# Kernel optimization log

Measured on AMD Instinct MI355X. Metric: run time of the kernel, lower is better.

The kernel has to match this reference:

```python
import jax, jax.numpy as jnp
import numpy as np
from jax import lax

SL, BS, D, H, T = 256, 64, 1024, 512, 17
BN_EPS = 1e-5


def setup_inputs() -> dict:
    key = jax.random.key(0)
    ks = jax.random.split(key, 16)
    k = 1.0 / np.sqrt(H)
    u = lambda kk, shape: jax.random.uniform(kk, shape, jnp.float32, -k, k)
    word_input = jax.random.normal(ks[0], (SL, BS, D), jnp.float32)
    lengths = jax.random.randint(ks[1], (BS,), SL // 2, SL + 1)
    mask = jnp.arange(SL)[:, None] < lengths[None, :]  # (SL, BS), first step all valid
    labels = jax.random.randint(ks[2], (SL, BS), 0, T)
    return dict(
        word_input=word_input, mask=mask, labels=labels,
        w_ih_f=u(ks[3], (4 * H, D)), w_hh_f=u(ks[4], (4 * H, H)),
        b_ih_f=u(ks[5], (4 * H,)), b_hh_f=u(ks[6], (4 * H,)),
        w_ih_b=u(ks[7], (4 * H, D)), w_hh_b=u(ks[8], (4 * H, H)),
        b_ih_b=u(ks[9], (4 * H,)), b_hh_b=u(ks[10], (4 * H,)),
        bn_gamma=jnp.ones((2 * H,), jnp.float32), bn_beta=jnp.zeros((2 * H,), jnp.float32),
        lin_w=u(ks[11], (T, 2 * H)), lin_b=u(ks[12], (T,)),
        crf_start=0.1 * jax.random.normal(ks[13], (T,), jnp.float32),
        crf_end=0.1 * jax.random.normal(ks[14], (T,), jnp.float32),
        crf_trans=0.1 * jax.random.normal(ks[15], (T, T), jnp.float32),
    )


def _lstm_dir(x, w_ih, w_hh, b_ih, b_hh, reverse):
    # x: (SL, BS, D); PyTorch gate order i, f, g, o
    B = x.shape[1]
    h0 = jnp.zeros((B, H), x.dtype)
    xg = jnp.einsum('sbd,gd->sbg', x, w_ih) + b_ih + b_hh  # precompute input projections

    def step(carry, xt):
        h, c = carry
        g = xt + h @ w_hh.T
        i, f, gg, o = jnp.split(g, 4, axis=-1)
        c = jax.nn.sigmoid(f) * c + jax.nn.sigmoid(i) * jnp.tanh(gg)
        h = jax.nn.sigmoid(o) * jnp.tanh(c)
        return (h, c), h

    _, hs = lax.scan(step, (h0, h0), xg, reverse=reverse)
    return hs  # (SL, BS, H)


def _crf_llh(E, y, m, start, end, trans):
    # E: (B, L, T) batch-first emissions; y: (B, L) int; m: (B, L) bool
    B = E.shape[0]
    mf = m.astype(E.dtype)
    b = jnp.arange(B)
    # numerator (gold path score)
    emit = jnp.take_along_axis(E, y[:, :, None], axis=2)[:, :, 0]  # (B, L)
    num = start[y[:, 0]] + emit[:, 0]
    tr = trans[y[:, :-1], y[:, 1:]]  # (B, L-1)
    num = num + jnp.sum(mf[:, 1:] * (tr + emit[:, 1:]), axis=1)
    last = jnp.sum(m.astype(jnp.int32), axis=1) - 1
    num = num + end[y[b, last]]
    # partition function via forward algorithm
    alpha0 = start + E[:, 0]  # (B, T)

    def step(alpha, inp):
        e_t, m_t = inp
        nxt = jax.nn.logsumexp(alpha[:, :, None] + trans[None], axis=1) + e_t
        return jnp.where(m_t[:, None], nxt, alpha), None

    alpha, _ = lax.scan(step, alpha0, (E[:, 1:].transpose(1, 0, 2), m[:, 1:].T))
    Z = jax.nn.logsumexp(alpha + end, axis=1)
    return jnp.sum(num - Z)


def _viterbi(E, m, start, end, trans):
    # E: (B, L, T); m: (B, L) bool -> padded tags (B, L)
    B = E.shape[0]
    b = jnp.arange(B)
    score0 = start + E[:, 0]  # (B, T)

    def fwd(score, inp):
        e_t, m_t = inp
        cand = score[:, :, None] + trans[None]  # (B, T, T)
        best_prev = jnp.argmax(cand, axis=1)  # (B, T)
        best = jnp.max(cand, axis=1) + e_t
        return jnp.where(m_t[:, None], best, score), best_prev

    final, history = lax.scan(fwd, score0, (E[:, 1:].transpose(1, 0, 2), m[:, 1:].T))
    last_tag = jnp.argmax(final + end, axis=1)  # (B,)

    def bwd(tag, inp):
        bp, m_t = inp
        prev = jnp.where(m_t, bp[b, tag], tag)
        return prev, tag

    tag0, tags_rest = lax.scan(bwd, last_tag, (history, m[:, 1:].T), reverse=True)
    tags = jnp.concatenate([tag0[None], tags_rest], axis=0).T  # (B, L)
    return jnp.where(m, tags, 0)


def _forward(word_input, mask, labels, w_ih_f, w_hh_f, b_ih_f, b_hh_f,
             w_ih_b, w_hh_b, b_ih_b, b_hh_b, bn_gamma, bn_beta, lin_w, lin_b,
             crf_start, crf_end, crf_trans):
    hf = _lstm_dir(word_input, w_ih_f, w_hh_f, b_ih_f, b_hh_f, reverse=False)
    hb = _lstm_dir(word_input, w_ih_b, w_hh_b, b_ih_b, b_hh_b, reverse=True)
    lstm_out = jnp.concatenate([hf, hb], axis=-1)  # (SL, BS, 2H)
    x = lstm_out.reshape(-1, 2 * H)
    mean = x.mean(0)
    var = x.var(0)  # biased, as in torch BN training normalization
    xn = (x - mean) / jnp.sqrt(var + BN_EPS) * bn_gamma + bn_beta
    logits = xn @ lin_w.T + lin_b  # (SL*BS, T)
    E = logits.reshape(SL, BS, T).transpose(1, 0, 2)  # batch-first (B, L, T)
    m = mask.T  # (B, L)
    loss = -_crf_llh(E, labels.T, m, crf_start, crf_end, crf_trans)
    preds = _viterbi(E, m, crf_start, crf_end, crf_trans)
    return loss, preds


def reference(word_input, mask, labels, w_ih_f, w_hh_f, b_ih_f, b_hh_f,
              w_ih_b, w_hh_b, b_ih_b, b_hh_b, bn_gamma, bn_beta, lin_w, lin_b,
              crf_start, crf_end, crf_trans):
    return _forward(word_input, mask, labels, w_ih_f, w_hh_f, b_ih_f, b_hh_f,
                    w_ih_b, w_hh_b, b_ih_b, b_hh_b, bn_gamma, bn_beta, lin_w, lin_b,
                    crf_start, crf_end, crf_trans)
```

## Files before the change

### kernel.cpp

```cpp
#include <hip/hip_runtime.h>
#include <hip/hip_bf16.h>
#include <math.h>

#define SL 256
#define BS 64
#define DI 1024
#define HH 512
#define TT 17
#define NR (SL*BS)
#define G4 (4*HH)
#define C2 (2*HH)
#define NBLK 128

__device__ __forceinline__ float sigm(float x) { return 1.f / (1.f + expf(-x)); }

typedef float vfloat4 __attribute__((ext_vector_type(4)));
typedef __attribute__((ext_vector_type(8))) short short8v;
typedef __attribute__((ext_vector_type(4))) float f32x4;

__device__ __forceinline__ void coh_load4(float4& d, const float* p) {
    asm volatile("global_load_dwordx4 %0, %1, off sc0 sc1" : "=v"(d) : "v"(p) : "memory");
}
__device__ __forceinline__ void coh_load4i(int4& d, const int* p) {
    asm volatile("global_load_dwordx4 %0, %1, off sc0 sc1" : "=v"(d) : "v"(p) : "memory");
}
__device__ __forceinline__ void coh_store4(const float4& d, float* p) {
    vfloat4 t; t.x = d.x; t.y = d.y; t.z = d.z; t.w = d.w;
    asm volatile("global_store_dwordx4 %0, %1, off sc0 sc1" :: "v"(p), "v"(t) : "memory");
}
__device__ __forceinline__ void wait_vm0() { asm volatile("s_waitcnt vmcnt(0)" ::: "memory"); }

__device__ __forceinline__ void split8(const float4& x0, const float4& x1,
                                       short8v& h, short8v& l)
{
    const float xs[8] = {x0.x, x0.y, x0.z, x0.w, x1.x, x1.y, x1.z, x1.w};
    #pragma unroll
    for (int j = 0; j < 8; ++j) {
        const uint u   = __float_as_uint(xs[j]);
        const float hf = __uint_as_float(u & 0xFFFF0000u);
        h[j] = (short)(u >> 16);
        const float lo = xs[j] - hf;
        const uint v   = __float_as_uint(lo);
        l[j] = (short)((v + 0x7FFFu + ((v >> 16) & 1u)) >> 16);
    }
}

__global__ __launch_bounds__(256) void gemm_xg_mfma(
    const float* __restrict__ A,
    const float* __restrict__ W,
    const float* __restrict__ b1,
    const float* __restrict__ b2,
    float* __restrict__ C)
{
    const int tid  = threadIdx.x;
    const int lane = tid & 63;
    const int w    = tid >> 6;
    const int wm   = w >> 1, wn = w & 1;
    const int m0   = blockIdx.y * 128 + wm * 64;
    const int n0   = blockIdx.x * 128 + wn * 64;
    const int lr   = lane & 15;
    const int lk   = (lane >> 4) * 8;

    const float* pA = A + (size_t)(m0 + lr) * DI + lk;
    const float* pB = W + (size_t)(n0 + lr) * DI + lk;

    f32x4 acc[4][4];
    #pragma unroll
    for (int i = 0; i < 4; i++)
        #pragma unroll
        for (int j = 0; j < 4; j++) {
            acc[i][j][0] = 0.f; acc[i][j][1] = 0.f;
            acc[i][j][2] = 0.f; acc[i][j][3] = 0.f;
        }

    for (int k0 = 0; k0 < DI; k0 += 32) {
        short8v ah[4], al[4], bh[4], bl[4];
        #pragma unroll
        for (int i = 0; i < 4; i++) {
            const float4 a0 = *(const float4*)(pA + (size_t)i * 16 * DI + k0);
            const float4 a1 = *(const float4*)(pA + (size_t)i * 16 * DI + k0 + 4);
            split8(a0, a1, ah[i], al[i]);
            const float4 b0 = *(const float4*)(pB + (size_t)i * 16 * DI + k0);
            const float4 b1v = *(const float4*)(pB + (size_t)i * 16 * DI + k0 + 4);
            split8(b0, b1v, bh[i], bl[i]);
        }
        #pragma unroll
        for (int i = 0; i < 4; i++)
            #pragma unroll
            for (int j = 0; j < 4; j++)
                acc[i][j] = __builtin_amdgcn_mfma_f32_16x16x32_bf16(ah[i], bh[j], acc[i][j], 0, 0, 0);
        #pragma unroll
        for (int i = 0; i < 4; i++)
            #pragma unroll
            for (int j = 0; j < 4; j++)
                acc[i][j] = __builtin_amdgcn_mfma_f32_16x16x32_bf16(ah[i], bl[j], acc[i][j], 0, 0, 0);
        #pragma unroll
        for (int i = 0; i < 4; i++)
            #pragma unroll
            for (int j = 0; j < 4; j++)
                acc[i][j] = __builtin_amdgcn_mfma_f32_16x16x32_bf16(al[i], bh[j], acc[i][j], 0, 0, 0);
    }

    #pragma unroll
    for (int j = 0; j < 4; j++) {
        const int n  = n0 + j * 16 + lr;
        const float bs = b1[n] + b2[n];
        const int u  = n & 511, g = n >> 9;
        const int s0 = u >> 2,  c = g * 4 + (u & 3);
        #pragma unroll
        for (int i = 0; i < 4; i++) {
            #pragma unroll
            for (int r = 0; r < 4; r++) {
                const int m  = m0 + i * 16 + (lane >> 4) * 4 + r;
                const int mt = m >> 6, mb = m & 63;
                C[((((size_t)s0 * SL + mt) * BS + mb) << 4) + c] = acc[i][j][r] + bs;
            }
        }
    }
}

__global__ __launch_bounds__(256) void pack_whh_v3(const float* __restrict__ whh,
                                                   float* __restrict__ wp)
{
    const int s = blockIdx.x;
    for (int idx = threadIdx.x; idx < 512 * 24; idx += 256) {
        const int k = idx / 24, c = idx % 24;
        float v = 0.f;
        if (c < 16) {
            const int g = c >> 2, uu = c & 3;
            v = whh[(size_t)(g * 512 + 4 * s + uu) * HH + k];
        }
        wp[(size_t)s * 12288 + idx] = v;
    }
}

__global__ __launch_bounds__(512) void init_flags(int* __restrict__ f)
{
    f[blockIdx.x * 512 + threadIdx.x] = 0;
}

__global__ __launch_bounds__(512, 2) void lstm_flag(
    const float* __restrict__ xg_f, const float* __restrict__ xg_b,
    const float* __restrict__ wp_f, const float* __restrict__ wp_b,
    float* __restrict__ Hf, float* __restrict__ Hb,
    int* __restrict__ flag_f, int* __restrict__ flag_b,
    float* __restrict__ out,
    int dir_base)
{
    __shared__ float w_s[512 * 24];
    __shared__ float hs[128 * 68];
    __shared__ float g_s[16 * 65];
    __shared__ float hpub[256];
    float* const part = hs;

    const int dir = dir_base + (blockIdx.x >> 7);
    const int s   = blockIdx.x & 127;
    const float* xg  = dir ? xg_b : xg_f;
    const float* wp  = dir ? wp_b : wp_f;
    float* Hbuf      = dir ? Hb : Hf;
    int*   flag      = dir ? flag_b : flag_f;
    const int reverse = dir;
    const int col_off = dir * HH;

    const int tid = threadIdx.x;
    const int ks  = tid >> 4;
    const int bt  = (tid >> 1) & 7;
    const int ct  = tid & 1;
    const int wv  = tid >> 6;

    {
        const float4* src = (const float4*)(wp + (size_t)s * 12288);
        float4* dst = (float4*)w_s;
        for (int i = tid; i < 3072; i += 512) dst[i] = src[i];
    }

    const float* xgs = xg + (size_t)s * (SL * 1024);
    float cst = 0.f;
    float4 r[4];
    float4 acc[8][2];

    for (int step = 0; step < SL; ++step) {
        const int t = reverse ? (SL - 1 - step) : step;
        const float myxg0 = xgs[t * 1024 + tid];
        const float myxg1 = xgs[t * 1024 + 512 + tid];

        if (step > 0) {
            if (tid < 32) {
                const int* fp = flag + (step - 1) * NBLK + tid * 4;
                int4 f;
                for (;;) {
                    coh_load4i(f, fp);
                    wait_vm0();
                    if (f.x & f.y & f.z & f.w) break;
                    __builtin_amdgcn_s_sleep(1);
                }
            }
            __syncthreads();

            const float* hsrc = Hbuf + ((step + 1) & 1) * (512 * 64);
            #pragma unroll
            for (int i = 0; i < 4; ++i)
                coh_load4(r[i], hsrc + (size_t)(i * 512 + tid) * 4);

            #pragma unroll
            for (int i = 0; i < 8; ++i) {
                acc[i][0] = make_float4(0.f, 0.f, 0.f, 0.f);
                acc[i][1] = make_float4(0.f, 0.f, 0.f, 0.f);
            }

            for (int kc = 0; kc < 4; ++kc) {
                if (kc) __syncthreads();
                wait_vm0();
                #pragma unroll
                for (int i = 0; i < 4; ++i) {
                    const int idx = i * 512 + tid;
                    const int k = idx >> 4, b4 = (idx & 15) * 4;
                    *(float4*)&hs[k * 68 + b4] = r[i];
                }
                __syncthreads();
                if (kc < 3) {
                    const float* base = hsrc + (size_t)(kc + 1) * 8192;
                    #pragma unroll
                    for (int i = 0; i < 4; ++i)
                        coh_load4(r[i], base + (size_t)(i * 512 + tid) * 4);
                }
                #pragma unroll
                for (int j = 0; j < 4; ++j) {
                    const int kk = ks + 32 * j;
                    const int kg = kc * 128 + kk;
                    const float4 w0 = *(const float4*)&w_s[kg * 24 + ct * 8];
                    const float4 w1 = *(const float4*)&w_s[kg * 24 + ct * 8 + 4];
                    const float* hp = &hs[kk * 68 + 8 * bt];
                    const float2 h01 = *(const float2*)(hp + 0);
                    const float2 h23 = *(const float2*)(hp + 2);
                    const float2 h45 = *(const float2*)(hp + 4);
                    const float2 h67 = *(const float2*)(hp + 6);
                    const float hv[8] = {h01.x, h01.y, h23.x, h23.y, h45.x, h45.y, h67.x, h67.y};
                    #pragma unroll
                    for (int i = 0; i < 8; ++i) {
                        acc[i][0].x = fmaf(hv[i], w0.x, acc[i][0].x);
                        acc[i][0].y = fmaf(hv[i], w0.y, acc[i][0].y);
                        acc[i][0].z = fmaf(hv[i], w0.z, acc[i][0].z);
                        acc[i][0].w = fmaf(hv[i], w0.w, acc[i][0].w);
                        acc[i][1].x = fmaf(hv[i], w1.x, acc[i][1].x);
                        acc[i][1].y = fmaf(hv[i], w1.y, acc[i][1].y);
                        acc[i][1].z = fmaf(hv[i], w1.z, acc[i][1].z);
                        acc[i][1].w = fmaf(hv[i], w1.w, acc[i][1].w);
                    }
                }
            }
            #pragma unroll
            for (int i = 0; i < 8; ++i)
                #pragma unroll
                for (int p = 0; p < 2; ++p) {
                    acc[i][p].x += __shfl_xor(acc[i][p].x, 16);
                    acc[i][p].y += __shfl_xor(acc[i][p].y, 16);
                    acc[i][p].z += __shfl_xor(acc[i][p].z, 16);
                    acc[i][p].w += __shfl_xor(acc[i][p].w, 16);
                    acc[i][p].x += __shfl_xor(acc[i][p].x, 32);
                    acc[i][p].y += __shfl_xor(acc[i][p].y, 32);
                    acc[i][p].z += __shfl_xor(acc[i][p].z, 32);
                    acc[i][p].w += __shfl_xor(acc[i][p].w, 32);
                }
            __syncthreads();
            if ((tid & 63) < 16) {
                #pragma unroll
                for (int i = 0; i < 8; ++i) {
                    const int base = wv * 1088 + (8 * bt + i) * 16 + ct * 8 + bt * 8;
                    *(float4*)&part[base + 0] = acc[i][0];
                    *(float4*)&part[base + 4] = acc[i][1];
                }
            }
            __syncthreads();
        }

        {
            float v0 = myxg0, v1 = myxg1;
            if (step > 0) {
                const int gA = tid, gB = tid + 512;
                const int iA = gA + 8 * (gA >> 7);
                const int iB = gB + 8 * (gB >> 7);
                #pragma unroll
                for (int w = 0; w < 8; ++w) {
                    v0 += part[w * 1088 + iA];
                    v1 += part[w * 1088 + iB];
                }
            }
            g_s[(tid & 15) * 65 + (tid >> 4)] = v0;
            {
                const int gB = tid + 512;
                g_s[(gB & 15) * 65 + (gB >> 4)] = v1;
            }
        }
        __syncthreads();

        if (tid < 256) {
            const int b = tid & 63, uu = tid >> 6;
            const float ig = sigm(g_s[(0  + uu) * 65 + b]);
            const float fg = sigm(g_s[(4  + uu) * 65 + b]);
            const float gg = tanhf(g_s[(8  + uu) * 65 + b]);
            const float og = sigm(g_s[(12 + uu) * 65 + b]);
            cst = fg * cst + ig * gg;
            hpub[tid] = og * tanhf(cst);
        }
        __syncthreads();
        if (tid < 16) {
            const float4 v = *(const float4*)&hpub[tid * 16];
            coh_store4(v, Hbuf + (step & 1) * (512 * 64) + s * 256 + tid * 16);
            *(float4*)(out + (size_t)(col_off + 4 * s + (tid >> 2)) * NR
                           + (size_t)t * 64 + (tid & 3) * 16) = v;
        }
        if (wv == 0) wait_vm0();
        __syncthreads();
        if (tid == 0)
            __hip_atomic_store(flag + step * NBLK + s, 1,
                               __ATOMIC_RELEASE, __HIP_MEMORY_SCOPE_AGENT);
    }
}

__global__ __launch_bounds__(256) void bn_stats(
    const float* __restrict__ X2, float* __restrict__ mean, float* __restrict__ istd)
{
    const int ch = blockIdx.x, tid = threadIdx.x;
    const float* base = X2 + (size_t)ch * NR;
    __shared__ float red[256];
    float s = 0.f;
    for (int i = tid * 4; i < NR; i += 1024) {
        const float4 v = *(const float4*)(base + i);
        s += v.x + v.y + v.z + v.w;
    }
    red[tid] = s; __syncthreads();
    for (int o = 128; o; o >>= 1) { if (tid < o) red[tid] += red[tid + o]; __syncthreads(); }
    const float mu = red[0] * (1.f / NR);
    __syncthreads();
    float vv = 0.f;
    for (int i = tid * 4; i < NR; i += 1024) {
        const float4 v = *(const float4*)(base + i);
        const float d0 = v.x - mu, d1 = v.y - mu, d2 = v.z - mu, d3 = v.w - mu;
        vv += d0 * d0 + d1 * d1 + d2 * d2 + d3 * d3;
    }
    red[tid] = vv; __syncthreads();
    for (int o = 128; o; o >>= 1) { if (tid < o) red[tid] += red[tid + o]; __syncthreads(); }
    if (tid == 0) { mean[ch] = mu; istd[ch] = rsqrtf(red[0] * (1.f / NR) + 1e-5f); }
}

__global__ void fold_lin(const float* __restrict__ lin_w, const float* __restrict__ lin_b,
                         const float* __restrict__ gamma, const float* __restrict__ beta,
                         const float* __restrict__ mean, const float* __restrict__ istd,
                         float* __restrict__ Wf, float* __restrict__ ct)
{
    const int t = blockIdx.x, tid = threadIdx.x;
    __shared__ float red[256];
    float acc = 0.f;
    for (int cc = tid; cc < C2; cc += 256) {
        const float w = lin_w[t * C2 + cc];
        const float g = gamma[cc] * istd[cc];
        Wf[t * C2 + cc] = w * g;
        acc = fmaf(beta[cc] - mean[cc] * g, w, acc);
    }
    red[tid] = acc; __syncthreads();
    for (int o = 128; o; o >>= 1) { if (tid < o) red[tid] += red[tid + o]; __syncthreads(); }
    if (tid == 0) ct[t] = red[0] + lin_b[t];
}

__global__ __launch_bounds__(256) void emit_logits(
    const float* __restrict__ X2, const float* __restrict__ Wf,
    const float* __restrict__ ct, float* __restrict__ E)
{
    __shared__ float ps[256 * TT];
    const int t = blockIdx.x;
    const int tid = threadIdx.x;
    const int b = tid & 63, p = tid >> 6;
    const float* xb = X2 + (size_t)t * 64 + b;

    float acc[TT];
    #pragma unroll
    for (int k = 0; k < TT; k++) acc[k] = 0.f;

    for (int c0 = p * 256; c0 < p * 256 + 256; c0 += 4) {
        const float x0 = xb[(size_t)(c0 + 0) * NR];
        const float x1 = xb[(size_t)(c0 + 1) * NR];
        const float x2 = xb[(size_t)(c0 + 2) * NR];
        const float x3 = xb[(size_t)(c0 + 3) * NR];
        #pragma unroll
        for (int k = 0; k < TT; k++) {
            const float4 w = *(const float4*)&Wf[k * C2 + c0];
            acc[k] = fmaf(x0, w.x, fmaf(x1, w.y, fmaf(x2, w.z, fmaf(x3, w.w, acc[k]))));
        }
    }
    #pragma unroll
    for (int k = 0; k < TT; k++) ps[tid * TT + k] = acc[k];
    __syncthreads();
    if (tid < 64) {
        float* Er = E + ((size_t)tid * SL + t) * TT;
        #pragma unroll
        for (int k = 0; k < TT; k++) {
            float v = ct[k];
            #pragma unroll
            for (int q = 0; q < 4; q++) v += ps[(q * 64 + tid) * TT + k];
            Er[k] = v;
        }
    }
}

__global__ __launch_bounds__(64) void crf_llh(
    const float* __restrict__ E, const int* __restrict__ mask,
    const int* __restrict__ labels, const float* __restrict__ startv,
    const float* __restrict__ endv, const float* __restrict__ trans,
    float* __restrict__ res)
{
    const int b = blockIdx.x, lane = threadIdx.x;
    __shared__ float tr[TT][TT];
    for (int i = lane; i < TT * TT; i += 64) tr[i / TT][i % TT] = trans[i];
    __syncthreads();
    const float* Eb = E + (size_t)b * SL * TT;
    const int j = (lane < TT) ? lane : 0;

    float alpha = -1e30f;
    if (lane < TT) alpha = startv[lane] + Eb[lane];

    float numacc = 0.f; int len = 0;
    for (int t = lane; t < SL; t += 64) {
        const int mt = mask[t * BS + b];
        len += (mt != 0);
        if (t >= 1 && mt) {
            const int yp = labels[(t - 1) * BS + b];
            const int yt = labels[t * BS + b];
            numacc += tr[yp][yt] + Eb[t * TT + yt];
        }
    }
    for (int off = 32; off; off >>= 1) {
        numacc += __shfl_xor(numacc, off);
        len += __shfl_xor(len, off);
    }

    for (int t = 1; t < SL; ++t) {
        const int mt = mask[t * BS + b];
        if (mt) {
            float av[TT];
            #pragma unroll
            for (int i = 0; i < TT; i++) av[i] = __shfl(alpha, i);
            const float e = (lane < TT) ? Eb[t * TT + lane] : 0.f;
            float mx = -1e30f;
            #pragma unroll
            for (int i = 0; i < TT; i++) mx = fmaxf(mx, av[i] + tr[i][j]);
            float ssum = 0.f;
            #pragma unroll
            for (int i = 0; i < TT; i++) ssum += expf(av[i] + tr[i][j] - mx);
            const float nxt = mx + logf(ssum) + e;
            if (lane < TT) alpha = nxt;
        }
    }
    float v = (lane < TT) ? alpha + endv[lane] : -1e30f;
    float mx = v;
    for (int off = 32; off; off >>= 1) mx = fmaxf(mx, __shfl_xor(mx, off));
    float se = (lane < TT) ? expf(v - mx) : 0.f;
    for (int off = 32; off; off >>= 1) se += __shfl_xor(se, off);
    const float Z = mx + logf(se);

    if (lane == 0) {
        const int y0 = labels[b];
        float num = startv[y0] + Eb[y0] + numacc;
        const int last = len - 1;
        const int yl = labels[last * BS + b];
        num += endv[yl];
        res[b] = num - Z;
    }
}

__global__ __launch_bounds__(64) void loss_reduce(const float* __restrict__ res, float* __restrict__ out)
{
    const int lane = threadIdx.x;
    float v = res[lane];
    for (int off = 32; off; off >>= 1) v += __shfl_xor(v, off);
    if (lane == 0) out[0] = -v;
}

__global__ __launch_bounds__(64) void viterbi(
    const float* __restrict__ E, const int* __restrict__ mask,
    const float* __restrict__ startv, const float* __restrict__ endv,
    const float* __restrict__ trans, float* __restrict__ preds)
{
    const int b = blockIdx.x, lane = threadIdx.x;
    __shared__ float tr[TT][TT];
    __shared__ unsigned char bp[SL][TT];
    for (int i = lane; i < TT * TT; i += 64) tr[i / TT][i % TT] = trans[i];
    __syncthreads();
    const float* Eb = E + (size_t)b * SL * TT;
    const int j = (lane < TT) ? lane : 0;

    float score = (lane < TT) ? startv[lane] + Eb[lane] : -1e30f;
    for (int t = 1; t < SL; ++t) {
        float av[TT];
        #pragma unroll
        for (int i = 0; i < TT; i++) av[i] = __shfl(score, i);
        float best = -1e30f; int bi = 0;
        #pragma unroll
        for (int i = 0; i < TT; i++) {
            const float cand = av[i] + tr[i][j];
            if (cand > best) { best = cand; bi = i; }
        }
        const int mt = mask[t * BS + b];
        if (lane < TT) {
            bp[t][lane] = (unsigned char)bi;
            if (mt) score = best + Eb[t * TT + lane];
        }
    }
    float v = (lane < TT) ? score + endv[lane] : -1e30f;
    float mx = v;
    for (int off = 32; off; off >>= 1) mx = fmaxf(mx, __shfl_xor(mx, off));
    unsigned long long ball = __ballot(v == mx);
    const int last_tag = __ffsll(ball) - 1;
    __syncthreads();

    if (lane == 0) {
        int tag = last_tag;
        float* pb = preds + (size_t)b * SL;
        for (int t = SL - 1; t >= 1; --t) {
            const int mt = mask[t * BS + b];
            pb[t] = mt ? (float)tag : 0.f;
            if (mt) tag = bp[t][tag];
        }
        pb[0] = mask[b] ? (float)tag : 0.f;
    }
}

extern "C" void kernel_launch(void* const* d_in, const int* in_sizes, int n_in,
                              void* d_out, int out_size, void* d_ws, size_t ws_size,
                              hipStream_t stream)
{
    const float* word    = (const float*)d_in[0];
    const int*   mask    = (const int*)  d_in[1];
    const int*   labels  = (const int*)  d_in[2];
    const float* w_ih_f  = (const float*)d_in[3];
    const float* w_hh_f  = (const float*)d_in[4];
    const float* b_ih_f  = (const float*)d_in[5];
    const float* b_hh_f  = (const float*)d_in[6];
    const float* w_ih_b  = (const float*)d_in[7];
    const float* w_hh_b  = (const float*)d_in[8];
    const float* b_ih_b  = (const float*)d_in[9];
    const float* b_hh_b  = (const float*)d_in[10];
    const float* gamma   = (const float*)d_in[11];
    const float* beta    = (const float*)d_in[12];
    const float* lin_w   = (const float*)d_in[13];
    const float* lin_b   = (const float*)d_in[14];
    const float* c_start = (const float*)d_in[15];
    const float* c_end   = (const float*)d_in[16];
    const float* c_trans = (const float*)d_in[17];
    float* out = (float*)d_out;
    (void)in_sizes; (void)n_in; (void)out_size;

    char* ws = (char*)d_ws;
    size_t off = 0;
    auto alloc = [&](size_t bytes) {
        void* p = ws + off;
        off += (bytes + 255) & ~(size_t)255;
        return p;
    };
    float* XG_F  = (float*)alloc((size_t)NR * G4 * 4);
    float* WPK_F = (float*)alloc((size_t)128 * 12288 * 4);
    float* WPK_B = (float*)alloc((size_t)128 * 12288 * 4);
    float* LOUT  = (float*)alloc((size_t)NR * C2 * 4);
    float* HB_F  = (float*)alloc((size_t)2 * 512 * 64 * 4);
    float* HB_B  = (float*)alloc((size_t)2 * 512 * 64 * 4);
    int*   FLAGS = (int*)  alloc((size_t)2 * SL * NBLK * 4);
    float* MEAN  = (float*)alloc(C2 * 4);
    float* ISTD  = (float*)alloc(C2 * 4);
    float* WF    = (float*)alloc(TT * C2 * 4);
    float* CT    = (float*)alloc(TT * 4);
    float* Ebuf  = (float*)alloc((size_t)BS * SL * TT * 4);
    float* RES   = (float*)alloc(BS * 4);
    float* XG_B  = (float*)alloc((size_t)NR * G4 * 4);
    const bool merged = (ws_size >= off);
    if (!merged) XG_B = XG_F;

    init_flags<<<128, 512, 0, stream>>>(FLAGS);
    pack_whh_v3<<<128, 256, 0, stream>>>(w_hh_f, WPK_F);
    pack_whh_v3<<<128, 256, 0, stream>>>(w_hh_b, WPK_B);

    if (merged) {
        gemm_xg_mfma<<<dim3(G4 / 128, NR / 128), 256, 0, stream>>>(word, w_ih_f, b_ih_f, b_hh_f, XG_F);
        gemm_xg_mfma<<<dim3(G4 / 128, NR / 128), 256, 0, stream>>>(word, w_ih_b, b_ih_b, b_hh_b, XG_B);
        lstm_flag<<<2 * NBLK, 512, 0, stream>>>(XG_F, XG_B, WPK_F, WPK_B, HB_F, HB_B,
                                                FLAGS, FLAGS + SL * NBLK, LOUT, 0);
    } else {
        gemm_xg_mfma<<<dim3(G4 / 128, NR / 128), 256, 0, stream>>>(word, w_ih_f, b_ih_f, b_hh_f, XG_F);
        lstm_flag<<<NBLK, 512, 0, stream>>>(XG_F, XG_B, WPK_F, WPK_B, HB_F, HB_B,
                                            FLAGS, FLAGS + SL * NBLK, LOUT, 0);
        gemm_xg_mfma<<<dim3(G4 / 128, NR / 128), 256, 0, stream>>>(word, w_ih_b, b_ih_b, b_hh_b, XG_F);
        lstm_flag<<<NBLK, 512, 0, stream>>>(XG_F, XG_B, WPK_F, WPK_B, HB_F, HB_B,
                                            FLAGS, FLAGS + SL * NBLK, LOUT, 1);
    }

    bn_stats<<<C2, 256, 0, stream>>>(LOUT, MEAN, ISTD);
    fold_lin<<<TT, 256, 0, stream>>>(lin_w, lin_b, gamma, beta, MEAN, ISTD, WF, CT);
    emit_logits<<<SL, 256, 0, stream>>>(LOUT, WF, CT, Ebuf);

    crf_llh<<<BS, 64, 0, stream>>>(Ebuf, mask, labels, c_start, c_end, c_trans, RES);
    loss_reduce<<<1, 64, 0, stream>>>(RES, out);
    viterbi<<<BS, 64, 0, stream>>>(Ebuf, mask, c_start, c_end, c_trans, out + 1);
}
```

Measured before the change: 8.762 ms.

## Stage split-bf16 GEMM tiles in LDS with prefetch and coalesced permuted stores

Rewrites the input-projection GEMM to load A and W tiles once into shared memory, split them into bf16 hi/lo there, and prefetch the next k-slice into registers while MFMAs run. The old version had each wave re-read and re-split its own operands from global memory. Each block's N columns are regrouped so that one block covers all four gates of 32 hidden units. The permuted output is then staged through LDS and written as contiguous float4 runs instead of scattered scalar stores. This adds barriers and LDS traffic, and may lower occupancy because of the 40 KB of shared memory per block.

Result: faster. 8.168 ms (-6.8%).

```diff
diff --git a/kernel.cpp b/kernel.cpp
--- a/kernel.cpp
+++ b/kernel.cpp
@@ -30,39 +30,63 @@
 }
 __device__ __forceinline__ void wait_vm0() { asm volatile("s_waitcnt vmcnt(0)" ::: "memory"); }
 
-__device__ __forceinline__ void split8(const float4& x0, const float4& x1,
-                                       short8v& h, short8v& l)
-{
-    const float xs[8] = {x0.x, x0.y, x0.z, x0.w, x1.x, x1.y, x1.z, x1.w};
-    #pragma unroll
-    for (int j = 0; j < 8; ++j) {
+__device__ __forceinline__ void split4(const float4& x, ushort4& h, ushort4& l)
+{
+    const float xs[4] = {x.x, x.y, x.z, x.w};
+    ushort hh[4], ll[4];
+    #pragma unroll
+    for (int j = 0; j < 4; ++j) {
         const uint u   = __float_as_uint(xs[j]);
         const float hf = __uint_as_float(u & 0xFFFF0000u);
-        h[j] = (short)(u >> 16);
+        hh[j] = (ushort)(u >> 16);
         const float lo = xs[j] - hf;
         const uint v   = __float_as_uint(lo);
-        l[j] = (short)((v + 0x7FFFu + ((v >> 16) & 1u)) >> 16);
-    }
-}
-
-__global__ __launch_bounds__(256) void gemm_xg_mfma(
+        ll[j] = (ushort)((v + 0x7FFFu + ((v >> 16) & 1u)) >> 16);
+    }
+    h.x = hh[0]; h.y = hh[1]; h.z = hh[2]; h.w = hh[3];
+    l.x = ll[0]; l.y = ll[1]; l.z = ll[2]; l.w = ll[3];
+}
+
+__global__ __launch_bounds__(256) void gemm_xg_v2(
     const float* __restrict__ A,
     const float* __restrict__ W,
     const float* __restrict__ b1,
     const float* __restrict__ b2,
     float* __restrict__ C)
 {
+    __shared__ ushort smem[4 * 128 * 40];
+    ushort* const Ah = smem;
+    ushort* const Al = smem + 1 * 5120;
+    ushort* const Bh = smem + 2 * 5120;
+    ushort* const Bl = smem + 3 * 5120;
+
     const int tid  = threadIdx.x;
     const int lane = tid & 63;
     const int w    = tid >> 6;
     const int wm   = w >> 1, wn = w & 1;
-    const int m0   = blockIdx.y * 128 + wm * 64;
-    const int n0   = blockIdx.x * 128 + wn * 64;
+    const int bx   = blockIdx.x;
+    const int by   = blockIdx.y;
+    const int m0   = by * 128;
+    const int u0   = bx * 32;
     const int lr   = lane & 15;
     const int lk   = (lane >> 4) * 8;
 
-    const float* pA = A + (size_t)(m0 + lr) * DI + lk;
-    const float* pB = W + (size_t)(n0 + lr) * DI + lk;
+    float bs[4];
+    #pragma unroll
+    for (int j = 0; j < 4; ++j) {
+        const int nl = wn * 64 + j * 16 + lr;
+        const int n  = (nl >> 5) * 512 + u0 + (nl & 31);
+        bs[j] = b1[n] + b2[n];
+    }
+
+    int arow[4], acol[4], brow[4];
+    #pragma unroll
+    for (int p = 0; p < 4; ++p) {
+        const int f = tid + p * 256;
+        arow[p] = f >> 3;
+        acol[p] = (f & 7) * 4;
+        brow[p] = (arow[p] >> 5) * 512 + u0 + (arow[p] & 31);
+    }
 
     f32x4 acc[4][4];
     #pragma unroll
@@ -73,16 +97,42 @@
             acc[i][j][2] = 0.f; acc[i][j][3] = 0.f;
         }
 
-    for (int k0 = 0; k0 < DI; k0 += 32) {
+    float4 ra[4], rb[4];
+    #pragma unroll
+    for (int p = 0; p < 4; ++p) {
+        ra[p] = *(const float4*)(A + (size_t)(m0 + arow[p]) * DI + acol[p]);
+        rb[p] = *(const float4*)(W + (size_t)brow[p] * DI + acol[p]);
+    }
+
+    for (int kt = 0; kt < DI; kt += 32) {
+        if (kt) __syncthreads();
+        #pragma unroll
+        for (int p = 0; p < 4; ++p) {
+            ushort4 h, l;
+            split4(ra[p], h, l);
+            *(ushort4*)&Ah[arow[p] * 40 + acol[p]] = h;
+            *(ushort4*)&Al[arow[p] * 40 + acol[p]] = l;
+            split4(rb[p], h, l);
+            *(ushort4*)&Bh[arow[p] * 40 + acol[p]] = h;
+            *(ushort4*)&Bl[arow[p] * 40 + acol[p]] = l;
+        }
+        __syncthreads();
+        if (kt + 32 < DI) {
+            #pragma unroll
+            for (int p = 0; p < 4; ++p) {
+                ra[p] = *(const float4*)(A + (size_t)(m0 + arow[p]) * DI + kt + 32 + acol[p]);
+                rb[p] = *(const float4*)(W + (size_t)brow[p] * DI + kt + 32 + acol[p]);
+            }
+        }
         short8v ah[4], al[4], bh[4], bl[4];
         #pragma unroll
-        for (int i = 0; i < 4; i++) {
-            const float4 a0 = *(const float4*)(pA + (size_t)i * 16 * DI + k0);
-            const float4 a1 = *(const float4*)(pA + (size_t)i * 16 * DI + k0 + 4);
-            split8(a0, a1, ah[i], al[i]);
-            const float4 b0 = *(const float4*)(pB + (size_t)i * 16 * DI + k0);
-            const float4 b1v = *(const float4*)(pB + (size_t)i * 16 * DI + k0 + 4);
-            split8(b0, b1v, bh[i], bl[i]);
+        for (int i = 0; i < 4; ++i) {
+            const int mr = wm * 64 + i * 16 + lr;
+            const int nr = wn * 64 + i * 16 + lr;
+            ah[i] = *(const short8v*)&Ah[mr * 40 + lk];
+            al[i] = *(const short8v*)&Al[mr * 40 + lk];
+            bh[i] = *(const short8v*)&Bh[nr * 40 + lk];
+            bl[i] = *(const short8v*)&Bl[nr * 40 + lk];
         }
         #pragma unroll
         for (int i = 0; i < 4; i++)
@@ -101,20 +151,33 @@
                 acc[i][j] = __builtin_amdgcn_mfma_f32_16x16x32_bf16(al[i], bh[j], acc[i][j], 0, 0, 0);
     }
 
-    #pragma unroll
-    for (int j = 0; j < 4; j++) {
-        const int n  = n0 + j * 16 + lr;
-        const float bs = b1[n] + b2[n];
-        const int u  = n & 511, g = n >> 9;
-        const int s0 = u >> 2,  c = g * 4 + (u & 3);
-        #pragma unroll
-        for (int i = 0; i < 4; i++) {
-            #pragma unroll
-            for (int r = 0; r < 4; r++) {
-                const int m  = m0 + i * 16 + (lane >> 4) * 4 + r;
-                const int mt = m >> 6, mb = m & 63;
-                C[((((size_t)s0 * SL + mt) * BS + mb) << 4) + c] = acc[i][j][r] + bs;
-            }
+    __syncthreads();
+    float* const Cl = (float*)smem;
+    const size_t s_base = (size_t)bx * 8;
+    #pragma unroll
+    for (int h = 0; h < 2; ++h) {
+        if (h) __syncthreads();
+        if (wm == h) {
+            #pragma unroll
+            for (int i = 0; i < 4; ++i)
+                #pragma unroll
+                for (int j = 0; j < 4; ++j) {
+                    const int nl = wn * 64 + j * 16 + lr;
+                    const int g = nl >> 5, du = nl & 31;
+                    const int s_rel = du >> 2, c = g * 4 + (du & 3);
+                    #pragma unroll
+                    for (int r = 0; r < 4; ++r) {
+                        const int ml = i * 16 + (lane >> 4) * 4 + r;
+                        Cl[s_rel * 1024 + ml * 16 + c] = acc[i][j][r] + bs[j];
+                    }
+                }
+        }
+        __syncthreads();
+        const int mt_g = by * 2 + h;
+        #pragma unroll
+        for (int ch = 0; ch < 8; ++ch) {
+            const float4 v = *(const float4*)&Cl[ch * 1024 + tid * 4];
+            *(float4*)(C + ((s_base + ch) * SL + mt_g) * 1024 + tid * 4) = v;
         }
     }
 }
@@ -579,15 +642,15 @@
     pack_whh_v3<<<128, 256, 0, stream>>>(w_hh_b, WPK_B);
 
     if (merged) {
-        gemm_xg_mfma<<<dim3(G4 / 128, NR / 128), 256, 0, stream>>>(word, w_ih_f, b_ih_f, b_hh_f, XG_F);
-        gemm_xg_mfma<<<dim3(G4 / 128, NR / 128), 256, 0, stream>>>(word, w_ih_b, b_ih_b, b_hh_b, XG_B);
+        gemm_xg_v2<<<dim3(16, 128), 256, 0, stream>>>(word, w_ih_f, b_ih_f, b_hh_f, XG_F);
+        gemm_xg_v2<<<dim3(16, 128), 256, 0, stream>>>(word, w_ih_b, b_ih_b, b_hh_b, XG_B);
         lstm_flag<<<2 * NBLK, 512, 0, stream>>>(XG_F, XG_B, WPK_F, WPK_B, HB_F, HB_B,
                                                 FLAGS, FLAGS + SL * NBLK, LOUT, 0);
     } else {
-        gemm_xg_mfma<<<dim3(G4 / 128, NR / 128), 256, 0, stream>>>(word, w_ih_f, b_ih_f, b_hh_f, XG_F);
+        gemm_xg_v2<<<dim3(16, 128), 256, 0, stream>>>(word, w_ih_f, b_ih_f, b_hh_f, XG_F);
         lstm_flag<<<NBLK, 512, 0, stream>>>(XG_F, XG_B, WPK_F, WPK_B, HB_F, HB_B,
                                             FLAGS, FLAGS + SL * NBLK, LOUT, 0);
-        gemm_xg_mfma<<<dim3(G4 / 128, NR / 128), 256, 0, stream>>>(word, w_ih_b, b_ih_b, b_hh_b, XG_F);
+        gemm_xg_v2<<<dim3(16, 128), 256, 0, stream>>>(word, w_ih_b, b_ih_b, b_hh_b, XG_F);
         lstm_flag<<<NBLK, 512, 0, stream>>>(XG_F, XG_B, WPK_F, WPK_B, HB_F, HB_B,
                                             FLAGS, FLAGS + SL * NBLK, LOUT, 1);
     }
```
